# Kernel optimization log

Hardware: AMD Instinct MI355X
Metric: run time of the kernel (lower is better)

Reference implementation:

```python
import jax, jax.numpy as jnp
import numpy as np
import math

B, N, D, H, FFN = 4, 2048, 512, 8, 2048
DK = D // H
EPS = 1e-5


def _layer_norm(x, g, b):
    mu = jnp.mean(x, axis=-1, keepdims=True)
    var = jnp.mean((x - mu) ** 2, axis=-1, keepdims=True)
    return (x - mu) * jax.lax.rsqrt(var + EPS) * g + b


def _rotate_half(x):
    h = x.shape[-1] // 2
    return jnp.concatenate([-x[..., h:], x[..., :h]], axis=-1)


def _rope(q, k, positions):
    # q, k: (B, H, N, DK); positions: (B, N) int
    inv_freq = 1.0 / (10000.0 ** (jnp.arange(0, DK, 2, dtype=jnp.float32) / DK))  # (DK/2,)
    ang = positions[:, None, :, None].astype(jnp.float32) * inv_freq  # (B,1,N,DK/2)
    cos = jnp.concatenate([jnp.cos(ang), jnp.cos(ang)], axis=-1)  # (B,1,N,DK)
    sin = jnp.concatenate([jnp.sin(ang), jnp.sin(ang)], axis=-1)
    q = q * cos + _rotate_half(q) * sin
    k = k * cos + _rotate_half(k) * sin
    return q, k


def setup_inputs() -> dict:
    key = jax.random.key(0)
    ks = jax.random.split(key, 16)
    s = 0.02
    x = jax.random.normal(ks[0], (B, N, D), dtype=jnp.float32)
    # backward-looking hop mask within jobs: random boolean with True diagonal
    m = jax.random.uniform(ks[1], (B, N, N)) < 0.1
    o2o_mask = m | jnp.eye(N, dtype=bool)[None]
    positions = jax.random.randint(ks[2], (B, N), 0, N)
    params = {
        'wq': jax.random.normal(ks[3], (D, D)) * s, 'bq': jnp.zeros((D,)),
        'wk': jax.random.normal(ks[4], (D, D)) * s, 'bk': jnp.zeros((D,)),
        'wv': jax.random.normal(ks[5], (D, D)) * s, 'bv': jnp.zeros((D,)),
        'wo': jax.random.normal(ks[6], (D, D)) * s, 'bo': jnp.zeros((D,)),
        'ln1_g': jnp.ones((D,)), 'ln1_b': jnp.zeros((D,)),
        'ln2_g': jnp.ones((D,)), 'ln2_b': jnp.zeros((D,)),
        'w1': jax.random.normal(ks[7], (D, FFN)) * s, 'b1': jnp.zeros((FFN,)),
        'w2': jax.random.normal(ks[8], (FFN, D)) * s, 'b2': jnp.zeros((D,)),
    }
    return {'x': x, 'o2o_mask': o2o_mask, 'positions': positions, **params}


def reference(x, o2o_mask, positions, wq, bq, wk, bk, wv, bv, wo, bo,
              ln1_g, ln1_b, ln2_g, ln2_b, w1, b1, w2, b2):
    residual = x
    xn = _layer_norm(x, ln1_g, ln1_b)
    q = (xn @ wq + bq).reshape(B, N, H, DK).transpose(0, 2, 1, 3)
    k = (xn @ wk + bk).reshape(B, N, H, DK).transpose(0, 2, 1, 3)
    v = (xn @ wv + bv).reshape(B, N, H, DK).transpose(0, 2, 1, 3)
    q, k = _rope(q, k, positions)
    scores = jnp.einsum('bhqd,bhkd->bhqk', q, k) / math.sqrt(DK)
    scores = jnp.where(o2o_mask[:, None], scores, -jnp.inf)
    attn = jax.nn.softmax(scores, axis=-1)
    attn = jnp.where(jnp.isnan(attn), 0.0, attn)  # fully-masked rows -> 0
    attn_out = jnp.einsum('bhqk,bhkd->bhqd', attn, v)
    attn_out = attn_out.transpose(0, 2, 1, 3).reshape(B, N, D)
    x = residual + (attn_out @ wo + bo)
    residual = x
    h = _layer_norm(x, ln2_g, ln2_b)
    h = jax.nn.relu(h @ w1 + b1) @ w2 + b2
    return residual + h
```

## Files before the change

### kernel.cpp

```cpp
#include <hip/hip_runtime.h>
#include <hip/hip_bf16.h>
#include <math.h>

typedef __attribute__((ext_vector_type(8))) __bf16 bf16x8;
typedef __attribute__((ext_vector_type(4))) __bf16 bf16x4;
typedef __attribute__((ext_vector_type(4))) float f32x4;

#define B_ 4
#define N_ 2048
#define D_ 512
#define H_ 8
#define DK_ 64
#define F_ 2048

__device__ __forceinline__ void async16(const __bf16* g, __bf16* l) {
  __builtin_amdgcn_global_load_lds((const __attribute__((address_space(1))) void*)g,
                                   (__attribute__((address_space(3))) void*)l, 16, 0, 0);
}

__global__ __launch_bounds__(256) void prep_bm_ln(const float* __restrict__ wq,
                                                  const float* __restrict__ wk,
                                                  const float* __restrict__ wv,
                                                  const float* __restrict__ wo,
                                                  const float* __restrict__ w1,
                                                  const float* __restrict__ w2,
                                                  const float* __restrict__ bq,
                                                  const float* __restrict__ bk,
                                                  const float* __restrict__ bv,
                                                  __bf16* __restrict__ wqkvt,
                                                  __bf16* __restrict__ wot,
                                                  __bf16* __restrict__ w1t,
                                                  __bf16* __restrict__ w2t,
                                                  float* __restrict__ bqkv,
                                                  const int* __restrict__ mask,
                                                  unsigned long long* __restrict__ bm,
                                                  const float* __restrict__ x,
                                                  const float* __restrict__ g,
                                                  const float* __restrict__ bb_,
                                                  __bf16* __restrict__ xnout) {
  __shared__ float t[64][65];
  const int id = blockIdx.x;
  if (id < 774) {
    if (id >= 768) {
      int i = (id - 768) * 256 + threadIdx.x;
      bqkv[i] = (i < 512) ? bq[i] : (i < 1024) ? bk[i - 512] : bv[i - 1024];
      return;
    }
    const float* in;
    __bf16* outp;
    int k0, n0, K, Nc;
    if (id < 256) {
      const float* src[4] = {wq, wk, wv, wo};
      __bf16* dst[4] = {wqkvt, wqkvt + 512 * 512, wqkvt + 1024 * 512, wot};
      int w = id >> 6, tl = id & 63;
      in = src[w]; outp = dst[w]; k0 = (tl & 7) * 64; n0 = (tl >> 3) * 64; K = 512; Nc = 512;
    } else if (id < 512) {
      int tl = id - 256;
      in = w1; outp = w1t; k0 = (tl & 7) * 64; n0 = (tl >> 3) * 64; K = 512; Nc = 2048;
    } else {
      int tl = id - 512;
      in = w2; outp = w2t; k0 = (tl & 31) * 64; n0 = (tl >> 5) * 64; K = 2048; Nc = 512;
    }
    const int c = threadIdx.x & 63, r4 = threadIdx.x >> 6;
#pragma unroll
    for (int p = 0; p < 16; p++) {
      int rr = p * 4 + r4;
      t[rr][c] = in[(size_t)(k0 + rr) * Nc + n0 + c];
    }
    __syncthreads();
#pragma unroll
    for (int p = 0; p < 16; p++) {
      int rr = p * 4 + r4;
      outp[(size_t)(n0 + rr) * K + k0 + c] = (__bf16)t[c][rr];
    }
  } else if (id < 774 + 8192) {
    const int bb = id - 774;
#pragma unroll
    for (int it = 0; it < 8; it++) {
      size_t tt = ((size_t)(it * 8192 + bb)) * 256 + threadIdx.x;
      int m = mask[tt];
      unsigned long long w = __ballot(m != 0);
      if ((threadIdx.x & 63) == 0) bm[tt >> 6] = w;
    }
  } else {
    int row = (id - 8966) * 4 + (threadIdx.x >> 6);
    int lane = threadIdx.x & 63;
    const float* xr = x + (size_t)row * D_ + lane * 8;
    float4 a0 = *(const float4*)xr;
    float4 a1 = *(const float4*)(xr + 4);
    float v[8] = {a0.x, a0.y, a0.z, a0.w, a1.x, a1.y, a1.z, a1.w};
    float s = 0.f;
#pragma unroll
    for (int i = 0; i < 8; i++) s += v[i];
#pragma unroll
    for (int off = 1; off < 64; off <<= 1) s += __shfl_xor(s, off);
    float mu = s * (1.f / D_);
    float q = 0.f;
#pragma unroll
    for (int i = 0; i < 8; i++) { float d = v[i] - mu; q += d * d; }
#pragma unroll
    for (int off = 1; off < 64; off <<= 1) q += __shfl_xor(q, off);
    float rs = rsqrtf(q * (1.f / D_) + 1e-5f);
    const float* gp = g + lane * 8;
    const float* bp = bb_ + lane * 8;
    alignas(16) __bf16 o[8];
#pragma unroll
    for (int i = 0; i < 8; i++) o[i] = (__bf16)((v[i] - mu) * rs * gp[i] + bp[i]);
    *(bf16x8*)(xnout + (size_t)row * D_ + lane * 8) = *(bf16x8*)o;
  }
}

__global__ __launch_bounds__(256) void ln_fwd(const float* __restrict__ x,
                                              const float* __restrict__ g,
                                              const float* __restrict__ b,
                                              __bf16* __restrict__ out) {
  int row = blockIdx.x * 4 + (threadIdx.x >> 6);
  int lane = threadIdx.x & 63;
  const float* xr = x + (size_t)row * D_ + lane * 8;
  float4 a0 = *(const float4*)xr;
  float4 a1 = *(const float4*)(xr + 4);
  float v[8] = {a0.x, a0.y, a0.z, a0.w, a1.x, a1.y, a1.z, a1.w};
  float s = 0.f;
#pragma unroll
  for (int i = 0; i < 8; i++) s += v[i];
#pragma unroll
  for (int off = 1; off < 64; off <<= 1) s += __shfl_xor(s, off);
  float mu = s * (1.f / D_);
  float q = 0.f;
#pragma unroll
  for (int i = 0; i < 8; i++) { float d = v[i] - mu; q += d * d; }
#pragma unroll
  for (int off = 1; off < 64; off <<= 1) q += __shfl_xor(q, off);
  float rs = rsqrtf(q * (1.f / D_) + 1e-5f);
  const float* gp = g + lane * 8;
  const float* bp = b + lane * 8;
  alignas(16) __bf16 o[8];
#pragma unroll
  for (int i = 0; i < 8; i++) o[i] = (__bf16)((v[i] - mu) * rs * gp[i] + bp[i]);
  *(bf16x8*)(out + (size_t)row * D_ + lane * 8) = *(bf16x8*)o;
}

__global__ __launch_bounds__(256) void rope_vtrans(const __bf16* __restrict__ qkv,
                                                   const int* __restrict__ pos,
                                                   __bf16* __restrict__ qo,
                                                   __bf16* __restrict__ ko,
                                                   __bf16* __restrict__ vt) {
  __shared__ __bf16 tl[64][65];
  const int id = blockIdx.x;
  if (id < 8192) {
    int t = id * 256 + threadIdx.x;
    int d = t & 31;
    int h = (t >> 5) & 7;
    int n = (t >> 8) & (N_ - 1);
    int b = t >> 19;
    const __bf16* base = qkv + (size_t)(b * N_ + n) * 1536 + h * 64 + d;
    float q1 = (float)base[0], q2 = (float)base[32];
    float k1 = (float)base[512], k2 = (float)base[544];
    float p = (float)pos[b * N_ + n];
    float inv = __expf(-(float)d * (9.210340371976184f / 32.f));
    float ang = p * inv;
    float sn, cs;
    sincosf(ang, &sn, &cs);
    const float SC = 0.18033688011112042f;
    size_t ob = ((size_t)(b * H_ + h) * N_ + n) * DK_ + d;
    qo[ob]      = (__bf16)((q1 * cs - q2 * sn) * SC);
    qo[ob + 32] = (__bf16)((q2 * cs + q1 * sn) * SC);
    ko[ob]      = (__bf16)(k1 * cs - k2 * sn);
    ko[ob + 32] = (__bf16)(k2 * cs + k1 * sn);
  } else {
    const int lin = id - 8192;
    const int n0 = (lin & 31) * 64, h = (lin >> 5) & 7, b = lin >> 8;
    const int c = threadIdx.x & 63, rr = threadIdx.x >> 6;
#pragma unroll
    for (int p = 0; p < 16; p++) {
      int i = p * 4 + rr;
      tl[i][c] = qkv[(size_t)(b * N_ + n0 + i) * 1536 + 1024 + h * 64 + c];
    }
    __syncthreads();
    size_t ob = (size_t)(b * H_ + h) * DK_ * N_;
#pragma unroll
    for (int p = 0; p < 16; p++) {
      int dd = p * 4 + rr;
      vt[ob + (size_t)dd * N_ + n0 + c] = tl[c][dd];
    }
  }
}

__device__ __forceinline__ int xcd_remap(int bid, int nwg) {
  return (bid & 7) * (nwg >> 3) + (bid >> 3);
}

template <int RELU, int OBF, int RES>
__global__ __launch_bounds__(256) void gemm_bt(const __bf16* __restrict__ A,
                                               const __bf16* __restrict__ Bt,
                                               const float* __restrict__ bias,
                                               const float* __restrict__ res,
                                               void* __restrict__ Cout,
                                               int M, int N, int K) {
  __shared__ __bf16 As[2][128 * 32];
  __shared__ __bf16 Bs[2][128 * 32];
  const int tid = threadIdx.x;
  const int lane = tid & 63;
  const int wave = tid >> 6;
  const int quad = lane >> 4;
  const int l16 = lane & 15;
  const int nwgx = gridDim.x;
  const int gl = xcd_remap(blockIdx.y * nwgx + blockIdx.x, nwgx * gridDim.y);
  const int m0 = (gl / nwgx) * 128;
  const int n0 = (gl % nwgx) * 128;
  const int wm = (wave >> 1) * 64;
  const int wn = (wave & 1) * 64;
  f32x4 acc[4][4] = {};

  const int c0 = tid, c1 = tid + 256;
  const int ar0 = c0 >> 2, ak0 = (c0 & 3) * 8;
  const int ar1 = c1 >> 2, ak1 = (c1 & 3) * 8;

  auto stage = [&](int k0, int buf) {
    async16(A + (size_t)(m0 + ar0) * K + k0 + ak0, As[buf] + c0 * 8);
    async16(A + (size_t)(m0 + ar1) * K + k0 + ak1, As[buf] + c1 * 8);
    async16(Bt + (size_t)(n0 + ar0) * K + k0 + ak0, Bs[buf] + c0 * 8);
    async16(Bt + (size_t)(n0 + ar1) * K + k0 + ak1, Bs[buf] + c1 * 8);
  };

  stage(0, 0);
  __syncthreads();
  const int niter = K >> 5;
  for (int it = 0; it < niter; it++) {
    const int buf = it & 1;
    if (it + 1 < niter) stage((it + 1) * 32, buf ^ 1);
    bf16x8 af[4], bf[4];
#pragma unroll
    for (int mi = 0; mi < 4; mi++)
      af[mi] = *(const bf16x8*)(As[buf] + (wm + mi * 16 + l16) * 32 + quad * 8);
#pragma unroll
    for (int ni = 0; ni < 4; ni++)
      bf[ni] = *(const bf16x8*)(Bs[buf] + (wn + ni * 16 + l16) * 32 + quad * 8);
#pragma unroll
    for (int mi = 0; mi < 4; mi++)
#pragma unroll
      for (int ni = 0; ni < 4; ni++)
        acc[mi][ni] = __builtin_amdgcn_mfma_f32_16x16x32_bf16(af[mi], bf[ni], acc[mi][ni], 0, 0, 0);
    __syncthreads();
  }
#pragma unroll
  for (int ni = 0; ni < 4; ni++) {
    const int col = n0 + wn + ni * 16 + l16;
    const float bv = bias[col];
#pragma unroll
    for (int mi = 0; mi < 4; mi++) {
#pragma unroll
      for (int r = 0; r < 4; r++) {
        const int row = m0 + wm + mi * 16 + quad * 4 + r;
        float v = acc[mi][ni][r] + bv;
        if (RES) v += res[(size_t)row * N + col];
        if (RELU) v = fmaxf(v, 0.f);
        if (OBF) ((__bf16*)Cout)[(size_t)row * N + col] = (__bf16)v;
        else     ((float*)Cout)[(size_t)row * N + col] = v;
      }
    }
  }
}

template <int RELU, int OBF, int RES>
__global__ __launch_bounds__(256) void gemm_bt64(const __bf16* __restrict__ A,
                                                 const __bf16* __restrict__ Bt,
                                                 const float* __restrict__ bias,
                                                 const float* __restrict__ res,
                                                 void* __restrict__ Cout,
                                                 int M, int N, int K) {
  __shared__ __bf16 As[2][128 * 32];
  __shared__ __bf16 Bs[2][64 * 32];
  const int tid = threadIdx.x;
  const int lane = tid & 63;
  const int wave = tid >> 6;
  const int quad = lane >> 4;
  const int l16 = lane & 15;
  const int nwgx = gridDim.x;
  const int gl = xcd_remap(blockIdx.y * nwgx + blockIdx.x, nwgx * gridDim.y);
  const int m0 = (gl / nwgx) * 128;
  const int n0 = (gl % nwgx) * 64;
  const int wm = wave * 32;
  f32x4 acc[2][4] = {};

  const int ar0 = tid >> 2, ak0 = (tid & 3) * 8;

  auto stage = [&](int k0, int buf) {
    async16(A + (size_t)(m0 + ar0) * K + k0 + ak0, As[buf] + tid * 8);
    async16(A + (size_t)(m0 + 64 + ar0) * K + k0 + ak0, As[buf] + (tid + 256) * 8);
    async16(Bt + (size_t)(n0 + ar0) * K + k0 + ak0, Bs[buf] + tid * 8);
  };

  stage(0, 0);
  __syncthreads();
  const int niter = K >> 5;
  for (int it = 0; it < niter; it++) {
    const int buf = it & 1;
    if (it + 1 < niter) stage((it + 1) * 32, buf ^ 1);
    bf16x8 af[2], bf[4];
#pragma unroll
    for (int mi = 0; mi < 2; mi++)
      af[mi] = *(const bf16x8*)(As[buf] + (wm + mi * 16 + l16) * 32 + quad * 8);
#pragma unroll
    for (int ni = 0; ni < 4; ni++)
      bf[ni] = *(const bf16x8*)(Bs[buf] + (ni * 16 + l16) * 32 + quad * 8);
#pragma unroll
    for (int mi = 0; mi < 2; mi++)
#pragma unroll
      for (int ni = 0; ni < 4; ni++)
        acc[mi][ni] = __builtin_amdgcn_mfma_f32_16x16x32_bf16(af[mi], bf[ni], acc[mi][ni], 0, 0, 0);
    __syncthreads();
  }
#pragma unroll
  for (int ni = 0; ni < 4; ni++) {
    const int col = n0 + ni * 16 + l16;
    const float bv = bias[col];
#pragma unroll
    for (int mi = 0; mi < 2; mi++) {
#pragma unroll
      for (int r = 0; r < 4; r++) {
        const int row = m0 + wm + mi * 16 + quad * 4 + r;
        float v = acc[mi][ni][r] + bv;
        if (RES) v += res[(size_t)row * N + col];
        if (RELU) v = fmaxf(v, 0.f);
        if (OBF) ((__bf16*)Cout)[(size_t)row * N + col] = (__bf16)v;
        else     ((float*)Cout)[(size_t)row * N + col] = v;
      }
    }
  }
}

__global__ __launch_bounds__(512, 4) void flash_attn(const __bf16* __restrict__ q,
                                                     const __bf16* __restrict__ k,
                                                     const __bf16* __restrict__ vt,
                                                     const unsigned long long* __restrict__ bm,
                                                     __bf16* __restrict__ out) {
  const int bid = blockIdx.x;
  const int gl = ((bid & 7) << 6) | (bid >> 3);
  const int qt = gl & 15;
  const int h = (gl >> 4) & 7;
  const int b = gl >> 7;
  const int tid = threadIdx.x;
  const int lane = tid & 63, wave = tid >> 6;
  const int quad = lane >> 4, l16 = lane & 15;
  __shared__ __bf16 Ks[3][64 * 64];
  __shared__ __bf16 Vs[3][64 * 64];
  __shared__ __bf16 P[8][16 * 68];
  const size_t bh = (size_t)b * H_ + h;
  const __bf16* qp = q + (bh * N_ + qt * 128 + wave * 16) * DK_;
  bf16x8 qf[2];
#pragma unroll
  for (int ks = 0; ks < 2; ks++)
    qf[ks] = *(const bf16x8*)(qp + l16 * DK_ + ks * 32 + quad * 8);
  const __bf16* kbase = k + bh * N_ * DK_;
  const __bf16* vbase = vt + bh * DK_ * N_;
  const int qrow0 = qt * 128 + wave * 16 + l16;
  const unsigned long long* bmr = bm + (size_t)(b * N_ + qrow0) * (N_ / 64);
  const int xo = l16 & 7;

  f32x4 oacc[4] = {};
  float lsum = 0.f;

  const int sr = tid >> 3;
  const int sj = (tid & 7) ^ (sr & 7);
  const __bf16* ksrc = kbase + sr * DK_ + sj * 8;
  const __bf16* vsrc = vbase + (size_t)sr * N_ + sj * 8;

  auto stage = [&](int kt, int buf) {
    async16(ksrc + (size_t)kt * 64 * DK_, Ks[buf] + tid * 8);
    async16(vsrc + kt * 64, Vs[buf] + tid * 8);
  };

  stage(0, 0);
  stage(1, 1);
  unsigned long long mw = bmr[0];
  asm volatile("s_waitcnt vmcnt(3)" ::: "memory");
  __builtin_amdgcn_s_barrier();
  __builtin_amdgcn_sched_barrier(0);

  for (int kt = 0; kt < 32; kt++) {
    const int buf = kt % 3;
    const int nstage = (kt + 2 < 32) ? kt + 2 : 31;
    stage(nstage, (kt + 2) % 3);
    const int nmask = (kt + 1 < 32) ? kt + 1 : 31;
    const unsigned long long mw_nxt = bmr[nmask];

    const unsigned long long mws = mw >> (quad * 4);
#pragma unroll
    for (int ci = 0; ci < 4; ci++) {
      const int row = ci * 16 + l16;
      bf16x8 kf0 = *(const bf16x8*)(Ks[buf] + (row * 8 + (quad ^ xo)) * 8);
      bf16x8 kf1 = *(const bf16x8*)(Ks[buf] + (row * 8 + ((4 + quad) ^ xo)) * 8);
      f32x4 a = {0.f, 0.f, 0.f, 0.f};
      a = __builtin_amdgcn_mfma_f32_16x16x32_bf16(kf0, qf[0], a, 0, 0, 0);
      a = __builtin_amdgcn_mfma_f32_16x16x32_bf16(kf1, qf[1], a, 0, 0, 0);
      const unsigned int nib = (unsigned int)(mws >> (ci * 16)) & 15u;
      bf16x4 pk;
#pragma unroll
      for (int r4 = 0; r4 < 4; r4++) {
        float in = ((nib >> r4) & 1u) ? a[r4] : -1e30f;
        float p;
        asm("v_exp_f32 %0, %1" : "=v"(p) : "v"(in));
        lsum += p;
        pk[r4] = (__bf16)p;
      }
      *(bf16x4*)(&P[wave][0] + l16 * 68 + ci * 16 + quad * 4) = pk;
    }
    bf16x8 pf0 = *(const bf16x8*)(&P[wave][0] + l16 * 68 + quad * 8);
    bf16x8 pf1 = *(const bf16x8*)(&P[wave][0] + l16 * 68 + 32 + quad * 8);
#pragma unroll
    for (int ni = 0; ni < 4; ni++) {
      const int row = ni * 16 + l16;
      bf16x8 vf0 = *(const bf16x8*)(Vs[buf] + (row * 8 + (quad ^ xo)) * 8);
      bf16x8 vf1 = *(const bf16x8*)(Vs[buf] + (row * 8 + ((4 + quad) ^ xo)) * 8);
      oacc[ni] = __builtin_amdgcn_mfma_f32_16x16x32_bf16(vf0, pf0, oacc[ni], 0, 0, 0);
      oacc[ni] = __builtin_amdgcn_mfma_f32_16x16x32_bf16(vf1, pf1, oacc[ni], 0, 0, 0);
    }
    asm volatile("s_waitcnt vmcnt(3)" ::: "memory");
    __builtin_amdgcn_s_barrier();
    __builtin_amdgcn_sched_barrier(0);
    mw = mw_nxt;
  }
  lsum += __shfl_xor(lsum, 16);
  lsum += __shfl_xor(lsum, 32);
  const float inv_l = (lsum > 0.f) ? 1.f / lsum : 0.f;
#pragma unroll
  for (int ni = 0; ni < 4; ni++) {
    bf16x4 ov;
#pragma unroll
    for (int r = 0; r < 4; r++) ov[r] = (__bf16)(oacc[ni][r] * inv_l);
    *(bf16x4*)(out + ((size_t)b * N_ + qrow0) * D_ + h * DK_ + ni * 16 + quad * 4) = ov;
  }
}

static constexpr size_t OFF_XN  = 0;
static constexpr size_t OFF_WT  = 8388608;
static constexpr size_t OFF_WO  = OFF_WT + 1572864;
static constexpr size_t OFF_W1  = OFF_WO + 524288;
static constexpr size_t OFF_W2  = OFF_W1 + 2097152;
static constexpr size_t OFF_BQ  = OFF_W2 + 2097152;
static constexpr size_t OFF_QKV = OFF_BQ + 6144;
static constexpr size_t OFF_QR  = OFF_QKV + 25165824;
static constexpr size_t OFF_KR  = OFF_QR + 8388608;
static constexpr size_t OFF_VT  = OFF_KR + 8388608;
static constexpr size_t OFF_AO  = OFF_VT + 8388608;
static constexpr size_t OFF_Y   = OFF_AO + 8388608;

extern "C" void kernel_launch(void* const* d_in, const int* in_sizes, int n_in,
                              void* d_out, int out_size, void* d_ws, size_t ws_size,
                              hipStream_t stream) {
  const float* x    = (const float*)d_in[0];
  const int*   mask = (const int*)d_in[1];
  const int*   pos  = (const int*)d_in[2];
  const float* wq   = (const float*)d_in[3];
  const float* bq   = (const float*)d_in[4];
  const float* wk   = (const float*)d_in[5];
  const float* bk   = (const float*)d_in[6];
  const float* wv   = (const float*)d_in[7];
  const float* bv   = (const float*)d_in[8];
  const float* wo   = (const float*)d_in[9];
  const float* bo   = (const float*)d_in[10];
  const float* ln1g = (const float*)d_in[11];
  const float* ln1b = (const float*)d_in[12];
  const float* ln2g = (const float*)d_in[13];
  const float* ln2b = (const float*)d_in[14];
  const float* w1   = (const float*)d_in[15];
  const float* b1   = (const float*)d_in[16];
  const float* w2   = (const float*)d_in[17];
  const float* b2   = (const float*)d_in[18];
  float* out = (float*)d_out;
  char* ws = (char*)d_ws;

  __bf16* xn    = (__bf16*)(ws + OFF_XN);
  __bf16* wqkvt = (__bf16*)(ws + OFF_WT);
  __bf16* wot   = (__bf16*)(ws + OFF_WO);
  __bf16* w1t   = (__bf16*)(ws + OFF_W1);
  __bf16* w2t   = (__bf16*)(ws + OFF_W2);
  float*  bqkv  = (float*)(ws + OFF_BQ);
  __bf16* qkv   = (__bf16*)(ws + OFF_QKV);
  __bf16* qr    = (__bf16*)(ws + OFF_QR);
  __bf16* kr    = (__bf16*)(ws + OFF_KR);
  __bf16* vt    = (__bf16*)(ws + OFF_VT);
  __bf16* attn  = (__bf16*)(ws + OFF_AO);
  float*  y     = (float*)(ws + OFF_Y);
  unsigned long long* bm = (unsigned long long*)(ws + OFF_Y);
  __bf16* hn    = xn;
  __bf16* h2    = qkv;

  dim3 b256(256);
  dim3 b512(512);
  prep_bm_ln<<<11014, b256, 0, stream>>>(wq, wk, wv, wo, w1, w2, bq, bk, bv,
                                         wqkvt, wot, w1t, w2t, bqkv,
                                         mask, bm, x, ln1g, ln1b, xn);
  gemm_bt<0, 1, 0><<<dim3(12, 64), b256, 0, stream>>>(xn, wqkvt, bqkv, nullptr, qkv, 8192, 1536, 512);
  rope_vtrans<<<9216, b256, 0, stream>>>(qkv, pos, qr, kr, vt);
  flash_attn<<<512, b512, 0, stream>>>(qr, kr, vt, bm, attn);
  gemm_bt64<0, 0, 1><<<dim3(8, 64), b256, 0, stream>>>(attn, wot, bo, x, y, 8192, 512, 512);
  ln_fwd<<<2048, b256, 0, stream>>>(y, ln2g, ln2b, hn);
  gemm_bt<1, 1, 0><<<dim3(16, 64), b256, 0, stream>>>(hn, w1t, b1, nullptr, h2, 8192, 2048, 512);
  gemm_bt64<0, 0, 1><<<dim3(8, 64), b256, 0, stream>>>(h2, w2t, b2, y, out, 8192, 512, 2048);
}
```

Before: 333.2 us.

## Fuse RoPE and Q scaling into QKV GEMM epilogue with precomputed cos/sin table

Adds a dedicated QKV GEMM whose epilogue applies bias, RoPE rotation and the Q softmax scale, writing Q and K directly in head-major layout. This removes the separate pass that re-read the Q/K portion of the qkv buffer. The sin/cos values are precomputed into a table inside the prep kernel and then read in the epilogue. The V transpose stays as its own smaller kernel. The epilogue writes are scattered 2-byte stores, which may be less coalesced than before.

```diff
diff --git a/kernel.cpp b/kernel.cpp
--- a/kernel.cpp
+++ b/kernel.cpp
@@ -37,7 +37,9 @@
                                                   const float* __restrict__ x,
                                                   const float* __restrict__ g,
                                                   const float* __restrict__ bb_,
-                                                  __bf16* __restrict__ xnout) {
+                                                  __bf16* __restrict__ xnout,
+                                                  const int* __restrict__ pos,
+                                                  float2* __restrict__ ctab) {
   __shared__ float t[64][65];
   const int id = blockIdx.x;
   if (id < 774) {
@@ -82,7 +84,7 @@
       unsigned long long w = __ballot(m != 0);
       if ((threadIdx.x & 63) == 0) bm[tt >> 6] = w;
     }
-  } else {
+  } else if (id < 11014) {
     int row = (id - 8966) * 4 + (threadIdx.x >> 6);
     int lane = threadIdx.x & 63;
     const float* xr = x + (size_t)row * D_ + lane * 8;
@@ -107,6 +109,14 @@
 #pragma unroll
     for (int i = 0; i < 8; i++) o[i] = (__bf16)((v[i] - mu) * rs * gp[i] + bp[i]);
     *(bf16x8*)(xnout + (size_t)row * D_ + lane * 8) = *(bf16x8*)o;
+  } else {
+    int e = (id - 11014) * 256 + threadIdx.x;
+    int row = e >> 5, d = e & 31;
+    float p = (float)pos[row];
+    float inv = __expf(-(float)d * (9.210340371976184f / 32.f));
+    float sn, cs;
+    sincosf(p * inv, &sn, &cs);
+    ctab[e] = make_float2(cs, sn);
   }
 }
 
@@ -140,54 +150,122 @@
   *(bf16x8*)(out + (size_t)row * D_ + lane * 8) = *(bf16x8*)o;
 }
 
-__global__ __launch_bounds__(256) void rope_vtrans(const __bf16* __restrict__ qkv,
-                                                   const int* __restrict__ pos,
-                                                   __bf16* __restrict__ qo,
-                                                   __bf16* __restrict__ ko,
-                                                   __bf16* __restrict__ vt) {
+__global__ __launch_bounds__(256) void vtrans(const __bf16* __restrict__ qkv,
+                                              __bf16* __restrict__ vt) {
   __shared__ __bf16 tl[64][65];
-  const int id = blockIdx.x;
-  if (id < 8192) {
-    int t = id * 256 + threadIdx.x;
-    int d = t & 31;
-    int h = (t >> 5) & 7;
-    int n = (t >> 8) & (N_ - 1);
-    int b = t >> 19;
-    const __bf16* base = qkv + (size_t)(b * N_ + n) * 1536 + h * 64 + d;
-    float q1 = (float)base[0], q2 = (float)base[32];
-    float k1 = (float)base[512], k2 = (float)base[544];
-    float p = (float)pos[b * N_ + n];
-    float inv = __expf(-(float)d * (9.210340371976184f / 32.f));
-    float ang = p * inv;
-    float sn, cs;
-    sincosf(ang, &sn, &cs);
-    const float SC = 0.18033688011112042f;
-    size_t ob = ((size_t)(b * H_ + h) * N_ + n) * DK_ + d;
-    qo[ob]      = (__bf16)((q1 * cs - q2 * sn) * SC);
-    qo[ob + 32] = (__bf16)((q2 * cs + q1 * sn) * SC);
-    ko[ob]      = (__bf16)(k1 * cs - k2 * sn);
-    ko[ob + 32] = (__bf16)(k2 * cs + k1 * sn);
-  } else {
-    const int lin = id - 8192;
-    const int n0 = (lin & 31) * 64, h = (lin >> 5) & 7, b = lin >> 8;
-    const int c = threadIdx.x & 63, rr = threadIdx.x >> 6;
-#pragma unroll
-    for (int p = 0; p < 16; p++) {
-      int i = p * 4 + rr;
-      tl[i][c] = qkv[(size_t)(b * N_ + n0 + i) * 1536 + 1024 + h * 64 + c];
-    }
-    __syncthreads();
-    size_t ob = (size_t)(b * H_ + h) * DK_ * N_;
-#pragma unroll
-    for (int p = 0; p < 16; p++) {
-      int dd = p * 4 + rr;
-      vt[ob + (size_t)dd * N_ + n0 + c] = tl[c][dd];
-    }
+  const int lin = blockIdx.x;
+  const int n0 = (lin & 31) * 64, h = (lin >> 5) & 7, b = lin >> 8;
+  const int c = threadIdx.x & 63, rr = threadIdx.x >> 6;
+#pragma unroll
+  for (int p = 0; p < 16; p++) {
+    int i = p * 4 + rr;
+    tl[i][c] = qkv[(size_t)(b * N_ + n0 + i) * 1536 + 1024 + h * 64 + c];
+  }
+  __syncthreads();
+  size_t ob = (size_t)(b * H_ + h) * DK_ * N_;
+#pragma unroll
+  for (int p = 0; p < 16; p++) {
+    int dd = p * 4 + rr;
+    vt[ob + (size_t)dd * N_ + n0 + c] = tl[c][dd];
   }
 }
 
 __device__ __forceinline__ int xcd_remap(int bid, int nwg) {
   return (bid & 7) * (nwg >> 3) + (bid >> 3);
+}
+
+__global__ __launch_bounds__(256) void gemm_qkv(const __bf16* __restrict__ A,
+                                                const __bf16* __restrict__ Bt,
+                                                const float* __restrict__ bias,
+                                                __bf16* __restrict__ qkvV,
+                                                __bf16* __restrict__ qr,
+                                                __bf16* __restrict__ kr,
+                                                const float2* __restrict__ ctab) {
+  constexpr int K = 512;
+  __shared__ __bf16 As[2][128 * 32];
+  __shared__ __bf16 Bs[2][128 * 32];
+  const int tid = threadIdx.x;
+  const int lane = tid & 63;
+  const int wave = tid >> 6;
+  const int quad = lane >> 4;
+  const int l16 = lane & 15;
+  const int gl = xcd_remap(blockIdx.y * 12 + blockIdx.x, 768);
+  const int m0 = (gl / 12) * 128;
+  const int n0 = (gl % 12) * 128;
+  const int wm = (wave >> 1) * 64;
+  const int wn = (wave & 1) * 64;
+  f32x4 acc[4][4] = {};
+
+  const int c0 = tid, c1 = tid + 256;
+  const int ar0 = c0 >> 2, ak0 = (c0 & 3) * 8;
+  const int ar1 = c1 >> 2, ak1 = (c1 & 3) * 8;
+
+  auto stage = [&](int k0, int buf) {
+    async16(A + (size_t)(m0 + ar0) * K + k0 + ak0, As[buf] + c0 * 8);
+    async16(A + (size_t)(m0 + ar1) * K + k0 + ak1, As[buf] + c1 * 8);
+    async16(Bt + (size_t)(n0 + ar0) * K + k0 + ak0, Bs[buf] + c0 * 8);
+    async16(Bt + (size_t)(n0 + ar1) * K + k0 + ak1, Bs[buf] + c1 * 8);
+  };
+
+  stage(0, 0);
+  __syncthreads();
+  const int niter = K >> 5;
+  for (int it = 0; it < niter; it++) {
+    const int buf = it & 1;
+    if (it + 1 < niter) stage((it + 1) * 32, buf ^ 1);
+    bf16x8 af[4], bf[4];
+#pragma unroll
+    for (int mi = 0; mi < 4; mi++)
+      af[mi] = *(const bf16x8*)(As[buf] + (wm + mi * 16 + l16) * 32 + quad * 8);
+#pragma unroll
+    for (int ni = 0; ni < 4; ni++)
+      bf[ni] = *(const bf16x8*)(Bs[buf] + (wn + ni * 16 + l16) * 32 + quad * 8);
+#pragma unroll
+    for (int mi = 0; mi < 4; mi++)
+#pragma unroll
+      for (int ni = 0; ni < 4; ni++)
+        acc[mi][ni] = __builtin_amdgcn_mfma_f32_16x16x32_bf16(af[mi], bf[ni], acc[mi][ni], 0, 0, 0);
+    __syncthreads();
+  }
+
+  if (n0 >= 1024) {
+#pragma unroll
+    for (int ni = 0; ni < 4; ni++) {
+      const int col = n0 + wn + ni * 16 + l16;
+      const float bv = bias[col];
+#pragma unroll
+      for (int mi = 0; mi < 4; mi++)
+#pragma unroll
+        for (int r = 0; r < 4; r++) {
+          const int row = m0 + wm + mi * 16 + quad * 4 + r;
+          qkvV[(size_t)row * 1536 + col] = (__bf16)(acc[mi][ni][r] + bv);
+        }
+    }
+  } else {
+    __bf16* outp = (n0 >= 512) ? kr : qr;
+    const float sc = (n0 >= 512) ? 1.0f : 0.18033688011112042f;
+    const int cl0 = n0 + wn + l16;
+    const float bl0 = bias[cl0],      bh0 = bias[cl0 + 32];
+    const float bl1 = bias[cl0 + 16], bh1 = bias[cl0 + 48];
+    const int h0 = (cl0 >> 6) & 7;
+    const int d0 = l16;
+#pragma unroll
+    for (int mi = 0; mi < 4; mi++)
+#pragma unroll
+      for (int r = 0; r < 4; r++) {
+        const int row = m0 + wm + mi * 16 + quad * 4 + r;
+        const int bb2 = row >> 11, nn = row & 2047;
+        const size_t ob = ((size_t)(bb2 * 8 + h0) * 2048 + nn) * 64;
+        const float2 ct0 = ctab[row * 32 + d0];
+        const float2 ct1 = ctab[row * 32 + d0 + 16];
+        const float vlo0 = acc[mi][0][r] + bl0, vhi0 = acc[mi][2][r] + bh0;
+        const float vlo1 = acc[mi][1][r] + bl1, vhi1 = acc[mi][3][r] + bh1;
+        outp[ob + d0]      = (__bf16)((vlo0 * ct0.x - vhi0 * ct0.y) * sc);
+        outp[ob + d0 + 32] = (__bf16)((vhi0 * ct0.x + vlo0 * ct0.y) * sc);
+        outp[ob + d0 + 16] = (__bf16)((vlo1 * ct1.x - vhi1 * ct1.y) * sc);
+        outp[ob + d0 + 48] = (__bf16)((vhi1 * ct1.x + vlo1 * ct1.y) * sc);
+      }
+  }
 }
 
 template <int RELU, int OBF, int RES>
@@ -484,16 +562,17 @@
   __bf16* attn  = (__bf16*)(ws + OFF_AO);
   float*  y     = (float*)(ws + OFF_Y);
   unsigned long long* bm = (unsigned long long*)(ws + OFF_Y);
+  float2* ctab  = (float2*)(ws + OFF_Y + 2097152);
   __bf16* hn    = xn;
   __bf16* h2    = qkv;
 
   dim3 b256(256);
   dim3 b512(512);
-  prep_bm_ln<<<11014, b256, 0, stream>>>(wq, wk, wv, wo, w1, w2, bq, bk, bv,
+  prep_bm_ln<<<12038, b256, 0, stream>>>(wq, wk, wv, wo, w1, w2, bq, bk, bv,
                                          wqkvt, wot, w1t, w2t, bqkv,
-                                         mask, bm, x, ln1g, ln1b, xn);
-  gemm_bt<0, 1, 0><<<dim3(12, 64), b256, 0, stream>>>(xn, wqkvt, bqkv, nullptr, qkv, 8192, 1536, 512);
-  rope_vtrans<<<9216, b256, 0, stream>>>(qkv, pos, qr, kr, vt);
+                                         mask, bm, x, ln1g, ln1b, xn, pos, ctab);
+  gemm_qkv<<<dim3(12, 64), b256, 0, stream>>>(xn, wqkvt, bqkv, qkv, qr, kr, ctab);
+  vtrans<<<1024, b256, 0, stream>>>(qkv, vt);
   flash_attn<<<512, b512, 0, stream>>>(qr, kr, vt, bm, attn);
   gemm_bt64<0, 0, 1><<<dim3(8, 64), b256, 0, stream>>>(attn, wot, bo, x, y, 8192, 512, 512);
   ln_fwd<<<2048, b256, 0, stream>>>(y, ln2g, ln2b, hn);
```

Measured after the change: 337.9 us. No clear change (+1.4%).
